# Optimization experiments

Measured on AMD Instinct MI355X. Metric: run time of the kernel, lower is better.

## Reference

```python
import jax, jax.numpy as jnp
import numpy as np

T, D, N, W = 8192, 768, 10000, 32  # tokens, hidden dim, num spans, max span width


def setup_inputs() -> dict:
    key = jax.random.key(0)
    k1, k2, k3, k4, k5 = jax.random.split(key, 5)
    sentence_embeddings = jax.random.normal(k1, (T, D), dtype=jnp.float32)
    lengths = jax.random.randint(k2, (N,), 1, W + 1)           # span lengths in [1, W]
    starts = jax.random.randint(k3, (N,), 0, T - W)
    ends = starts + lengths - 1                                 # inclusive end, < T
    sentence_spans = jnp.stack([starts, ends], axis=1).astype(jnp.int32)
    Wq = (jax.random.normal(k4, (D, D), dtype=jnp.float32) / np.sqrt(D).astype(np.float32))
    bq = jax.random.normal(k5, (D,), dtype=jnp.float32) * 0.01
    return {"sentence_embeddings": sentence_embeddings,
            "sentence_spans": sentence_spans,
            "Wq": Wq, "bq": bq}


def reference(sentence_embeddings, sentence_spans, Wq, bq):
    # Padded + masked batched version of the per-span loop:
    #   span_emb = emb[s:e+1]; q = span_emb @ Wq.T + bq
    #   w = softmax(q @ span_emb.T, dim=1); out = (w @ span_emb).sum(0)
    starts = sentence_spans[:, 0]                               # [N]
    lengths = sentence_spans[:, 1] - starts + 1                 # inclusive end -> length
    offs = jnp.arange(W)
    pos = starts[:, None] + offs[None, :]                       # [N, W] token indices
    valid = offs[None, :] < lengths[:, None]                    # [N, W] in-span mask
    pos = jnp.clip(pos, 0, sentence_embeddings.shape[0] - 1)
    span_emb = sentence_embeddings[pos]                         # [N, W, D] ragged gather
    span_emb = jnp.where(valid[:, :, None], span_emb, 0.0)
    query = jnp.einsum('nwd,ed->nwe', span_emb, Wq) + bq        # [N, W, D]
    scores = jnp.einsum('nqd,nkd->nqk', query, span_emb)        # [N, W, W]
    scores = jnp.where(valid[:, None, :], scores, -jnp.inf)     # mask pad keys (softmax dim=1)
    weights = jax.nn.softmax(scores, axis=-1)
    attn = jnp.einsum('nqk,nkd->nqd', weights, span_emb)        # [N, W, D]
    attn = jnp.where(valid[:, :, None], attn, 0.0)              # drop pad query rows
    return attn.sum(axis=1)                                     # [N, D] == torch.sum(attention, dim=0) per span
```

## Files before the change

### kernel.cpp

```cpp
#include <hip/hip_runtime.h>
#include <hip/hip_bf16.h>
#include <cstddef>
#include <cstdint>

constexpr int Tt = 8192;
constexpr int Dd = 768;
constexpr int Nn = 10000;
constexpr int Ww = 32;

typedef __bf16 bf16x8 __attribute__((ext_vector_type(8)));
typedef __bf16 bf16x4 __attribute__((ext_vector_type(4)));
typedef _Float16 half8v __attribute__((ext_vector_type(8)));
typedef _Float16 half4v __attribute__((ext_vector_type(4)));
typedef float f32x4 __attribute__((ext_vector_type(4)));

#define MFMA16(a, b, c) __builtin_amdgcn_mfma_f32_16x16x32_bf16((a), (b), (c), 0, 0, 0)
#define MFMAH(a, b, c) __builtin_amdgcn_mfma_f32_16x16x32_f16((a), (b), (c), 0, 0, 0)

__global__ __launch_bounds__(256) void conv_f16_kernel(const float* __restrict__ emb,
                                                       const float* __restrict__ Wq,
                                                       _Float16* __restrict__ Ef,
                                                       _Float16* __restrict__ Wf) {
    const int nE = (Tt * Dd) / 4;
    const int nW = (Dd * Dd) / 4;
    const int i = blockIdx.x * 256 + threadIdx.x;
    if (i < nE) {
        const float4 v = reinterpret_cast<const float4*>(emb)[i];
        half4v o;
        o[0] = (_Float16)v.x; o[1] = (_Float16)v.y;
        o[2] = (_Float16)v.z; o[3] = (_Float16)v.w;
        reinterpret_cast<half4v*>(Ef)[i] = o;
    } else {
        const int j = i - nE;
        if (j < nW) {
            const float4 v = reinterpret_cast<const float4*>(Wq)[j];
            half4v o;
            o[0] = (_Float16)v.x; o[1] = (_Float16)v.y;
            o[2] = (_Float16)v.z; o[3] = (_Float16)v.w;
            reinterpret_cast<half4v*>(Wf)[j] = o;
        }
    }
}

template <bool LO>
__global__ __launch_bounds__(256) void conv_kernel(const float* __restrict__ src,
                                                   __bf16* __restrict__ h,
                                                   __bf16* __restrict__ l, int n4) {
    const int i = blockIdx.x * 256 + threadIdx.x;
    if (i >= n4) return;
    const float4 v = reinterpret_cast<const float4*>(src)[i];
    bf16x4 oh, ol;
    oh[0] = (__bf16)v.x; oh[1] = (__bf16)v.y; oh[2] = (__bf16)v.z; oh[3] = (__bf16)v.w;
    reinterpret_cast<bf16x4*>(h)[i] = oh;
    if (LO) {
        ol[0] = (__bf16)(v.x - (float)oh[0]);
        ol[1] = (__bf16)(v.y - (float)oh[1]);
        ol[2] = (__bf16)(v.z - (float)oh[2]);
        ol[3] = (__bf16)(v.w - (float)oh[3]);
        reinterpret_cast<bf16x4*>(l)[i] = ol;
    }
}

__global__ __launch_bounds__(256) void zero_kernel(int* __restrict__ p, int n) {
    const int i = blockIdx.x * 256 + threadIdx.x;
    if (i < n) p[i] = 0;
}

__global__ __launch_bounds__(256) void hist_kernel(const int* __restrict__ spans,
                                                   int* __restrict__ hist) {
    const int i = blockIdx.x * 256 + threadIdx.x;
    if (i < Nn) atomicAdd(&hist[spans[2 * i]], 1);
}

__global__ __launch_bounds__(256) void scan_kernel(int* __restrict__ hist) {
    __shared__ int part[256];
    const int t = threadIdx.x;
    int vals[32];
    int sum = 0;
#pragma unroll
    for (int i = 0; i < 32; ++i) { vals[i] = hist[t * 32 + i]; sum += vals[i]; }
    part[t] = sum;
    __syncthreads();
    for (int off = 1; off < 256; off <<= 1) {
        const int v = (t >= off) ? part[t - off] : 0;
        __syncthreads();
        part[t] += v;
        __syncthreads();
    }
    int run = (t == 0) ? 0 : part[t - 1];
#pragma unroll
    for (int i = 0; i < 32; ++i) { const int v = vals[i]; hist[t * 32 + i] = run; run += v; }
}

__global__ __launch_bounds__(256) void scatter_kernel(const int* __restrict__ spans,
                                                      int* __restrict__ offs,
                                                      int* __restrict__ perm) {
    const int i = blockIdx.x * 256 + threadIdx.x;
    if (i < Nn) {
        const int p = atomicAdd(&offs[spans[2 * i]], 1);
        perm[p] = i;
    }
}

template <bool SPLIT>
__global__ __launch_bounds__(256) void qproj_kernel(const float* __restrict__ emb,
                                                    const float* __restrict__ Wq,
                                                    const float* __restrict__ bq,
                                                    __bf16* __restrict__ Qh,
                                                    __bf16* __restrict__ Ql) {
    __shared__ float As[64][32];
    __shared__ float Bs[64][32];
    const int tid = threadIdx.x;
    const int tx = tid & 15;
    const int ty = tid >> 4;
    const int m0 = blockIdx.x * 64;
    const int n0 = blockIdx.y * 64;

    float acc[4][4] = {};

    for (int kc = 0; kc < Dd; kc += 32) {
#pragma unroll
        for (int i = 0; i < 2; ++i) {
            const int f   = tid + i * 256;
            const int row = f >> 3;
            const int c4  = f & 7;
            const int ph  = (c4 + (row >> 2)) & 7;
            *reinterpret_cast<float4*>(&As[row][ph * 4]) =
                *reinterpret_cast<const float4*>(&emb[(size_t)(m0 + row) * Dd + kc + c4 * 4]);
            *reinterpret_cast<float4*>(&Bs[row][ph * 4]) =
                *reinterpret_cast<const float4*>(&Wq[(size_t)(n0 + row) * Dd + kc + c4 * 4]);
        }
        __syncthreads();
#pragma unroll
        for (int d4 = 0; d4 < 8; ++d4) {
            float4 av[4], bv[4];
#pragma unroll
            for (int r = 0; r < 4; ++r)
                av[r] = *reinterpret_cast<const float4*>(&As[ty * 4 + r][((d4 + ty) & 7) * 4]);
#pragma unroll
            for (int c = 0; c < 4; ++c)
                bv[c] = *reinterpret_cast<const float4*>(&Bs[tx * 4 + c][((d4 + tx) & 7) * 4]);
#pragma unroll
            for (int r = 0; r < 4; ++r)
#pragma unroll
                for (int c = 0; c < 4; ++c) {
                    acc[r][c] += av[r].x * bv[c].x;
                    acc[r][c] += av[r].y * bv[c].y;
                    acc[r][c] += av[r].z * bv[c].z;
                    acc[r][c] += av[r].w * bv[c].w;
                }
        }
        __syncthreads();
    }
#pragma unroll
    for (int r = 0; r < 4; ++r) {
        bf16x4 oh, ol;
#pragma unroll
        for (int c = 0; c < 4; ++c) {
            const float v = acc[r][c] + bq[n0 + tx * 4 + c];
            const __bf16 h = (__bf16)v;
            oh[c] = h;
            if (SPLIT) ol[c] = (__bf16)(v - (float)h);
        }
        const size_t off = (size_t)(m0 + ty * 4 + r) * Dd + n0 + tx * 4;
        *reinterpret_cast<bf16x4*>(&Qh[off]) = oh;
        if (SPLIT) *reinterpret_cast<bf16x4*>(&Ql[off]) = ol;
    }
}

__global__ __launch_bounds__(256) void qproj_f16_kernel(const _Float16* __restrict__ Ef,
                                                        const _Float16* __restrict__ Wf,
                                                        const float* __restrict__ bq,
                                                        _Float16* __restrict__ Qf) {
    __shared__ __align__(16) _Float16 As[128 * 64];
    __shared__ __align__(16) _Float16 Bs[96 * 64];

    const int tid  = threadIdx.x;
    const int wave = tid >> 6;
    const int lane = tid & 63;

    const int b   = blockIdx.x;
    const int xcd = b & 7;
    const int li  = b >> 3;
    const int mt  = xcd * 8 + (li >> 3);
    const int nt  = li & 7;
    const int m0 = mt * 128;
    const int n0 = nt * 96;
    const int wm = (wave & 1) * 64;
    const int wn = (wave >> 1) * 48;
    const int fr = lane & 15;
    const int kg = lane >> 4;

    int ar[4], ao[4];
#pragma unroll
    for (int i = 0; i < 4; ++i) {
        const int s = tid + i * 256;
        ar[i] = s >> 3;
        ao[i] = ((s & 7) ^ (ar[i] & 7)) * 8;
    }
    int br[3], bo[3];
#pragma unroll
    for (int i = 0; i < 3; ++i) {
        const int s = tid + i * 256;
        br[i] = s >> 3;
        bo[i] = ((s & 7) ^ (br[i] & 7)) * 8;
    }

    f32x4 acc[4][3] = {};

    for (int kc = 0; kc < Dd; kc += 64) {
        half8v ra[4], rb[3];
#pragma unroll
        for (int i = 0; i < 4; ++i)
            ra[i] = *reinterpret_cast<const half8v*>(&Ef[(size_t)(m0 + ar[i]) * Dd + kc + ao[i]]);
#pragma unroll
        for (int i = 0; i < 3; ++i)
            rb[i] = *reinterpret_cast<const half8v*>(&Wf[(size_t)(n0 + br[i]) * Dd + kc + bo[i]]);
        __syncthreads();
#pragma unroll
        for (int i = 0; i < 4; ++i)
            *reinterpret_cast<half8v*>(&As[(tid + i * 256) * 8]) = ra[i];
#pragma unroll
        for (int i = 0; i < 3; ++i)
            *reinterpret_cast<half8v*>(&Bs[(tid + i * 256) * 8]) = rb[i];
        __syncthreads();

#pragma unroll
        for (int step = 0; step < 2; ++step) {
            const int g = kg + 4 * step;
            half8v a[4], bb[3];
#pragma unroll
            for (int r = 0; r < 4; ++r) {
                const int R = wm + r * 16 + fr;
                a[r] = *reinterpret_cast<const half8v*>(&As[R * 64 + (g ^ (R & 7)) * 8]);
            }
#pragma unroll
            for (int c = 0; c < 3; ++c) {
                const int R = wn + c * 16 + fr;
                bb[c] = *reinterpret_cast<const half8v*>(&Bs[R * 64 + (g ^ (R & 7)) * 8]);
            }
#pragma unroll
            for (int r = 0; r < 4; ++r)
#pragma unroll
                for (int c = 0; c < 3; ++c)
                    acc[r][c] = MFMAH(a[r], bb[c], acc[r][c]);
        }
    }

#pragma unroll
    for (int c = 0; c < 3; ++c) {
        const int ocol = n0 + wn + c * 16 + fr;
        const float bqv = bq[ocol];
#pragma unroll
        for (int r = 0; r < 4; ++r)
#pragma unroll
            for (int j = 0; j < 4; ++j) {
                const int orow = m0 + wm + r * 16 + kg * 4 + j;
                Qf[(size_t)orow * Dd + ocol] = (_Float16)(acc[r][c][j] + bqv);
            }
    }
}

__global__ __launch_bounds__(256) void span_attn_win_kernel(const _Float16* __restrict__ Ef,
                                                            const int* __restrict__ spans,
                                                            const _Float16* __restrict__ Qf,
                                                            const int* __restrict__ perm,
                                                            float* __restrict__ out) {
    constexpr int WR = 48, CH = 128, ST = 136, NCH = Dd / CH;
    __shared__ __align__(16) _Float16 Qs[WR * ST];
    __shared__ __align__(16) _Float16 Es[WR * ST];

    const int tid  = threadIdx.x;
    const int wave = tid >> 6;
    const int lane = tid & 63;

    const int b     = blockIdx.x;
    const int bp    = (b & 7) * 313 + (b >> 3);
    const int slot0 = bp * 4;
    const int slot  = slot0 + wave;
    const bool active = slot < Nn;

    int s0 = perm[slot0 < Nn ? slot0 : (Nn - 1)];
    if ((unsigned)s0 >= (unsigned)Nn) s0 = 0;
    int s = active ? perm[slot] : s0;
    if ((unsigned)s >= (unsigned)Nn) s = 0;

    const int w0    = spans[2 * s0];
    const int start = spans[2 * s];
    const int L     = spans[2 * s + 1] - start + 1;
    const bool big  = L > 16;
    const int sl    = start - w0;
    const bool inwin = active && sl >= 0 && sl <= (WR - 32);

    const int row = lane & 15;
    const int kq  = lane >> 4;

    const size_t gq = (size_t)(start + row) * Dd + kq * 8;

    f32x4 acc00 = {0.f, 0.f, 0.f, 0.f};
    f32x4 acc01 = {0.f, 0.f, 0.f, 0.f};
    f32x4 acc10 = {0.f, 0.f, 0.f, 0.f};
    f32x4 acc11 = {0.f, 0.f, 0.f, 0.f};

    for (int c = 0; c < NCH; ++c) {
        const int c0 = c * CH;
        __syncthreads();
#pragma unroll
        for (int i = 0; i < 3; ++i) {
            const int seg = tid + i * 256;
            const int r  = seg >> 4;
            const int cs = seg & 15;
            const int gr = w0 + r < Tt ? w0 + r : Tt - 1;
            const size_t ga = (size_t)gr * Dd + c0 + cs * 8;
            *reinterpret_cast<half8v*>(&Qs[r * ST + cs * 8]) =
                *reinterpret_cast<const half8v*>(&Qf[ga]);
            *reinterpret_cast<half8v*>(&Es[r * ST + cs * 8]) =
                *reinterpret_cast<const half8v*>(&Ef[ga]);
        }
        __syncthreads();

        if (inwin) {
            const int ab = (sl + row) * ST + kq * 8;
#pragma unroll
            for (int j = 0; j < 4; ++j) {
                const int o = j * 32;
                const half8v a0 = *reinterpret_cast<const half8v*>(&Qs[ab + o]);
                const half8v b0 = *reinterpret_cast<const half8v*>(&Es[ab + o]);
                acc00 = MFMAH(a0, b0, acc00);
                if (big) {
                    const half8v a1 = *reinterpret_cast<const half8v*>(&Qs[ab + 16 * ST + o]);
                    const half8v b1 = *reinterpret_cast<const half8v*>(&Es[ab + 16 * ST + o]);
                    acc01 = MFMAH(a0, b1, acc01);
                    acc10 = MFMAH(a1, b0, acc10);
                    acc11 = MFMAH(a1, b1, acc11);
                }
            }
        } else if (active) {
#pragma unroll
            for (int j = 0; j < 4; ++j) {
                const int o = c0 + j * 32;
                const half8v a0 = *reinterpret_cast<const half8v*>(&Qf[gq + o]);
                const half8v b0 = *reinterpret_cast<const half8v*>(&Ef[gq + o]);
                acc00 = MFMAH(a0, b0, acc00);
                if (big) {
                    const half8v a1 = *reinterpret_cast<const half8v*>(&Qf[gq + 16 * Dd + o]);
                    const half8v b1 = *reinterpret_cast<const half8v*>(&Ef[gq + 16 * Dd + o]);
                    acc01 = MFMAH(a0, b1, acc01);
                    acc10 = MFMAH(a1, b0, acc10);
                    acc11 = MFMAH(a1, b1, acc11);
                }
            }
        }
    }

    const float NEG = -1e30f;
    const bool kv0 = row < L;
    const bool kv1 = (16 + row) < L;
    float cA, cB;
    {
        float w00[4], w01[4], w10[4], w11[4];
#pragma unroll
        for (int r = 0; r < 4; ++r) {
            float m = kv0 ? acc00[r] : NEG;
            if (big) m = fmaxf(m, kv1 ? acc01[r] : NEG);
#pragma unroll
            for (int st = 1; st <= 8; st <<= 1) m = fmaxf(m, __shfl_xor(m, st));
            const float e0 = kv0 ? __expf(acc00[r] - m) : 0.f;
            const float e1 = (big && kv1) ? __expf(acc01[r] - m) : 0.f;
            float sum = e0 + e1;
#pragma unroll
            for (int st = 1; st <= 8; st <<= 1) sum += __shfl_xor(sum, st);
            const float inv = 1.f / sum;
            const bool qv = (kq * 4 + r) < L;
            w00[r] = qv ? e0 * inv : 0.f;
            w01[r] = qv ? e1 * inv : 0.f;
            if (big) {
                float mh = kv0 ? acc10[r] : NEG;
                mh = fmaxf(mh, kv1 ? acc11[r] : NEG);
#pragma unroll
                for (int st = 1; st <= 8; st <<= 1) mh = fmaxf(mh, __shfl_xor(mh, st));
                const float f0 = kv0 ? __expf(acc10[r] - mh) : 0.f;
                const float f1 = kv1 ? __expf(acc11[r] - mh) : 0.f;
                float sh = f0 + f1;
#pragma unroll
                for (int st = 1; st <= 8; st <<= 1) sh += __shfl_xor(sh, st);
                const float invh = 1.f / sh;
                const bool qvh = (16 + kq * 4 + r) < L;
                w10[r] = qvh ? f0 * invh : 0.f;
                w11[r] = qvh ? f1 * invh : 0.f;
            }
        }
        float pa = w00[0] + w00[1] + w00[2] + w00[3];
        float pb = 0.f;
        if (big) {
            pa += w10[0] + w10[1] + w10[2] + w10[3];
            pb = w01[0] + w01[1] + w01[2] + w01[3] +
                 w11[0] + w11[1] + w11[2] + w11[3];
        }
        pa += __shfl_xor(pa, 16);
        pa += __shfl_xor(pa, 32);
        if (big) {
            pb += __shfl_xor(pb, 16);
            pb += __shfl_xor(pb, 32);
        }
        cA = pa;
        cB = pb;
    }

    if (active) {
        f32x4 o[3] = {};
        const int KP = (L + 3) & ~3;
        const _Float16* ebase = Ef + (size_t)start * Dd + lane * 4;
        for (int k = 0; k < KP; k += 4) {
            float cv[4];
            half4v ev[4][3];
#pragma unroll
            for (int j = 0; j < 4; ++j) {
                const int kk = k + j;
                cv[j] = (kk < 16) ? __shfl(cA, kk) : __shfl(cB, kk - 16);
#pragma unroll
                for (int i = 0; i < 3; ++i)
                    ev[j][i] = *reinterpret_cast<const half4v*>(ebase + (size_t)kk * Dd + i * 256);
            }
#pragma unroll
            for (int j = 0; j < 4; ++j)
#pragma unroll
                for (int i = 0; i < 3; ++i) {
                    o[i][0] += cv[j] * (float)ev[j][i][0];
                    o[i][1] += cv[j] * (float)ev[j][i][1];
                    o[i][2] += cv[j] * (float)ev[j][i][2];
                    o[i][3] += cv[j] * (float)ev[j][i][3];
                }
        }
#pragma unroll
        for (int i = 0; i < 3; ++i)
            *reinterpret_cast<f32x4*>(&out[(size_t)s * Dd + i * 256 + lane * 4]) = o[i];
    }
}

template <bool SPLIT, bool SORTED>
__global__ __launch_bounds__(256) void span_attn_g_kernel(const __bf16* __restrict__ Eb,
                                                          const int* __restrict__ spans,
                                                          const __bf16* __restrict__ Qh,
                                                          const __bf16* __restrict__ Ql,
                                                          const int* __restrict__ perm,
                                                          float* __restrict__ out) {
    const int wave = threadIdx.x >> 6;
    const int lane = threadIdx.x & 63;

    int s;
    bool active;
    if (SORTED) {
        const int b    = blockIdx.x;
        const int bp   = (b & 7) * 313 + (b >> 3);
        const int slot = bp * 4 + wave;
        active = slot < Nn;
        int sv = active ? perm[slot] : 0;
        if ((unsigned)sv >= (unsigned)Nn) sv = 0;
        s = sv;
    } else {
        s = blockIdx.x * 4 + wave;
        active = true;
    }

    const int start = spans[2 * s];
    const int L     = spans[2 * s + 1] - start + 1;
    const bool big  = L > 16;

    const int row = lane & 15;
    const int kq  = lane >> 4;

    const size_t rbase = (size_t)(start + row) * Dd + kq * 8;
    const __bf16* qh0 = Qh + rbase;
    const __bf16* eb0 = Eb + rbase;
    const __bf16* ql0 = SPLIT ? (Ql + rbase) : nullptr;

    f32x4 acc00 = {0.f, 0.f, 0.f, 0.f};
    f32x4 acc01 = {0.f, 0.f, 0.f, 0.f};
    f32x4 acc10 = {0.f, 0.f, 0.f, 0.f};
    f32x4 acc11 = {0.f, 0.f, 0.f, 0.f};

    if (!big) {
        for (int kc = 0; kc < Dd; kc += 128) {
            bf16x8 A[4], B[4], AL[4];
#pragma unroll
            for (int j = 0; j < 4; ++j) {
                const int o = kc + j * 32;
                A[j] = *reinterpret_cast<const bf16x8*>(qh0 + o);
                B[j] = *reinterpret_cast<const bf16x8*>(eb0 + o);
                if (SPLIT) AL[j] = *reinterpret_cast<const bf16x8*>(ql0 + o);
            }
#pragma unroll
            for (int j = 0; j < 4; ++j) {
                acc00 = MFMA16(A[j], B[j], acc00);
                if (SPLIT) acc00 = MFMA16(AL[j], B[j], acc00);
            }
        }
    } else {
        for (int kc = 0; kc < Dd; kc += 64) {
            bf16x8 A0[2], A1[2], B0[2], B1[2], AL0[2], AL1[2];
#pragma unroll
            for (int j = 0; j < 2; ++j) {
                const int o = kc + j * 32;
                A0[j] = *reinterpret_cast<const bf16x8*>(qh0 + o);
                A1[j] = *reinterpret_cast<const bf16x8*>(qh0 + 16 * Dd + o);
                B0[j] = *reinterpret_cast<const bf16x8*>(eb0 + o);
                B1[j] = *reinterpret_cast<const bf16x8*>(eb0 + 16 * Dd + o);
                if (SPLIT) {
                    AL0[j] = *reinterpret_cast<const bf16x8*>(ql0 + o);
                    AL1[j] = *reinterpret_cast<const bf16x8*>(ql0 + 16 * Dd + o);
                }
            }
#pragma unroll
            for (int j = 0; j < 2; ++j) {
                acc00 = MFMA16(A0[j], B0[j], acc00);
                acc01 = MFMA16(A0[j], B1[j], acc01);
                acc10 = MFMA16(A1[j], B0[j], acc10);
                acc11 = MFMA16(A1[j], B1[j], acc11);
                if (SPLIT) {
                    acc00 = MFMA16(AL0[j], B0[j], acc00);
                    acc01 = MFMA16(AL0[j], B1[j], acc01);
                    acc10 = MFMA16(AL1[j], B0[j], acc10);
                    acc11 = MFMA16(AL1[j], B1[j], acc11);
                }
            }
        }
    }

    const float NEG = -1e30f;
    const bool kv0 = row < L;
    const bool kv1 = (16 + row) < L;
    float cA, cB;
    {
        float w00[4], w01[4], w10[4], w11[4];
#pragma unroll
        for (int r = 0; r < 4; ++r) {
            float m = kv0 ? acc00[r] : NEG;
            if (big) m = fmaxf(m, kv1 ? acc01[r] : NEG);
#pragma unroll
            for (int st = 1; st <= 8; st <<= 1) m = fmaxf(m, __shfl_xor(m, st));
            const float e0 = kv0 ? __expf(acc00[r] - m) : 0.f;
            const float e1 = (big && kv1) ? __expf(acc01[r] - m) : 0.f;
            float sum = e0 + e1;
#pragma unroll
            for (int st = 1; st <= 8; st <<= 1) sum += __shfl_xor(sum, st);
            const float inv = 1.f / sum;
            const bool qv = (kq * 4 + r) < L;
            w00[r] = qv ? e0 * inv : 0.f;
            w01[r] = qv ? e1 * inv : 0.f;
            if (big) {
                float mh = kv0 ? acc10[r] : NEG;
                mh = fmaxf(mh, kv1 ? acc11[r] : NEG);
#pragma unroll
                for (int st = 1; st <= 8; st <<= 1) mh = fmaxf(mh, __shfl_xor(mh, st));
                const float f0 = kv0 ? __expf(acc10[r] - mh) : 0.f;
                const float f1 = kv1 ? __expf(acc11[r] - mh) : 0.f;
                float sh = f0 + f1;
#pragma unroll
                for (int st = 1; st <= 8; st <<= 1) sh += __shfl_xor(sh, st);
                const float invh = 1.f / sh;
                const bool qvh = (16 + kq * 4 + r) < L;
                w10[r] = qvh ? f0 * invh : 0.f;
                w11[r] = qvh ? f1 * invh : 0.f;
            }
        }
        float pa = w00[0] + w00[1] + w00[2] + w00[3];
        float pb = 0.f;
        if (big) {
            pa += w10[0] + w10[1] + w10[2] + w10[3];
            pb = w01[0] + w01[1] + w01[2] + w01[3] +
                 w11[0] + w11[1] + w11[2] + w11[3];
        }
        pa += __shfl_xor(pa, 16);
        pa += __shfl_xor(pa, 32);
        if (big) {
            pb += __shfl_xor(pb, 16);
            pb += __shfl_xor(pb, 32);
        }
        cA = pa;
        cB = pb;
    }

    if (active) {
        f32x4 o[3] = {};
        const int KP = (L + 3) & ~3;
        const __bf16* ebase = Eb + (size_t)start * Dd + lane * 4;
        for (int k = 0; k < KP; k += 4) {
            float cv[4];
            bf16x4 ev[4][3];
#pragma unroll
            for (int j = 0; j < 4; ++j) {
                const int kk = k + j;
                cv[j] = (kk < 16) ? __shfl(cA, kk) : __shfl(cB, kk - 16);
#pragma unroll
                for (int i = 0; i < 3; ++i)
                    ev[j][i] = *reinterpret_cast<const bf16x4*>(ebase + (size_t)kk * Dd + i * 256);
            }
#pragma unroll
            for (int j = 0; j < 4; ++j)
#pragma unroll
                for (int i = 0; i < 3; ++i) {
                    o[i][0] += cv[j] * (float)ev[j][i][0];
                    o[i][1] += cv[j] * (float)ev[j][i][1];
                    o[i][2] += cv[j] * (float)ev[j][i][2];
                    o[i][3] += cv[j] * (float)ev[j][i][3];
                }
        }
#pragma unroll
        for (int i = 0; i < 3; ++i)
            *reinterpret_cast<f32x4*>(&out[(size_t)s * Dd + i * 256 + lane * 4]) = o[i];
    }
}

extern "C" void kernel_launch(void* const* d_in, const int* in_sizes, int n_in,
                              void* d_out, int out_size, void* d_ws, size_t ws_size,
                              hipStream_t stream) {
    const float* emb   = (const float*)d_in[0];
    const int*   spans = (const int*)d_in[1];
    const float* Wq    = (const float*)d_in[2];
    const float* bq    = (const float*)d_in[3];
    float*       out   = (float*)d_out;

    const size_t TD = (size_t)Tt * Dd;
    const size_t DD = (size_t)Dd * Dd;
    const size_t intBytes = (size_t)(8192 + 10016) * sizeof(int);
    auto align16 = [](size_t x) { return (x + 15) & ~(size_t)15; };

    const size_t needMain = align16((2 * TD + DD) * 2) + intBytes;
    const size_t needB = align16(3 * TD * 2) + intBytes;
    const size_t needC = 3 * TD * 2;

    if (ws_size >= needMain) {
        char* base = (char*)d_ws;
        _Float16* Qf = (_Float16*)base;
        _Float16* Ef = (_Float16*)(base + TD * 2);
        _Float16* Wf = (_Float16*)(base + 2 * TD * 2);
        int* hist = (int*)(base + align16((2 * TD + DD) * 2));
        int* perm = hist + 8192;

        const int convBlocks = (int)((TD / 4 + DD / 4) / 256);
        conv_f16_kernel<<<convBlocks, 256, 0, stream>>>(emb, Wq, Ef, Wf);
        zero_kernel<<<32, 256, 0, stream>>>(hist, 8192);
        hist_kernel<<<40, 256, 0, stream>>>(spans, hist);
        scan_kernel<<<1, 256, 0, stream>>>(hist);
        scatter_kernel<<<40, 256, 0, stream>>>(spans, hist, perm);
        qproj_f16_kernel<<<512, 256, 0, stream>>>(Ef, Wf, bq, Qf);
        span_attn_win_kernel<<<2504, 256, 0, stream>>>(Ef, spans, Qf, perm, out);
    } else if (ws_size >= needB) {
        __bf16* w = (__bf16*)d_ws;
        __bf16* Qh = w;
        __bf16* Ql = w + TD;
        __bf16* Eh = w + 2 * TD;
        int* hist = (int*)((char*)d_ws + align16(3 * TD * 2));
        int* perm = hist + 8192;

        conv_kernel<false><<<(int)(TD / 4 / 256), 256, 0, stream>>>(emb, Eh, nullptr, (int)(TD / 4));
        zero_kernel<<<32, 256, 0, stream>>>(hist, 8192);
        hist_kernel<<<40, 256, 0, stream>>>(spans, hist);
        scan_kernel<<<1, 256, 0, stream>>>(hist);
        scatter_kernel<<<40, 256, 0, stream>>>(spans, hist, perm);
        qproj_kernel<true><<<dim3(Tt / 64, Dd / 64), 256, 0, stream>>>(emb, Wq, bq, Qh, Ql);
        span_attn_g_kernel<true, true><<<2504, 256, 0, stream>>>(Eh, spans, Qh, Ql, perm, out);
    } else if (ws_size >= needC) {
        __bf16* w = (__bf16*)d_ws;
        __bf16* Qh = w;
        __bf16* Ql = w + TD;
        __bf16* Eh = w + 2 * TD;
        conv_kernel<false><<<(int)(TD / 4 / 256), 256, 0, stream>>>(emb, Eh, nullptr, (int)(TD / 4));
        qproj_kernel<true><<<dim3(Tt / 64, Dd / 64), 256, 0, stream>>>(emb, Wq, bq, Qh, Ql);
        span_attn_g_kernel<true, false><<<2500, 256, 0, stream>>>(Eh, spans, Qh, Ql, nullptr, out);
    } else {
        __bf16* w = (__bf16*)d_ws;
        __bf16* Qh = w;
        __bf16* Eh = w + TD;
        conv_kernel<false><<<(int)(TD / 4 / 256), 256, 0, stream>>>(emb, Eh, nullptr, (int)(TD / 4));
        qproj_kernel<false><<<dim3(Tt / 64, Dd / 64), 256, 0, stream>>>(emb, Wq, bq, Qh, nullptr);
        span_attn_g_kernel<false, false><<<2500, 256, 0, stream>>>(Eh, spans, Qh, nullptr, nullptr, out);
    }
}
```

Baseline: 155.6 us.

## Fuse conversion, span sort and Q projection into one prep kernel

Replaces six prep launches (fp16 conversion, zero, histogram, scan, scatter, Q projection) with a single heterogeneous kernel. Block 0 builds the sorted span permutation in shared memory, blocks 1-512 compute the Q projection directly from fp32 inputs with on-the-fly fp16 conversion, and the remaining blocks convert the embeddings. This removes launch gaps and the separate Wq/E fp16 round trip, at the cost of the GEMM re-reading fp32 data. It also drops the unused intermediate fallback path.

```diff
diff --git a/kernel.cpp b/kernel.cpp
--- a/kernel.cpp
+++ b/kernel.cpp
@@ -17,28 +17,329 @@
 #define MFMA16(a, b, c) __builtin_amdgcn_mfma_f32_16x16x32_bf16((a), (b), (c), 0, 0, 0)
 #define MFMAH(a, b, c) __builtin_amdgcn_mfma_f32_16x16x32_f16((a), (b), (c), 0, 0, 0)
 
-__global__ __launch_bounds__(256) void conv_f16_kernel(const float* __restrict__ emb,
-                                                       const float* __restrict__ Wq,
-                                                       _Float16* __restrict__ Ef,
-                                                       _Float16* __restrict__ Wf) {
-    const int nE = (Tt * Dd) / 4;
-    const int nW = (Dd * Dd) / 4;
-    const int i = blockIdx.x * 256 + threadIdx.x;
-    if (i < nE) {
+__global__ __launch_bounds__(256) void prep_kernel(const float* __restrict__ emb,
+                                                   const float* __restrict__ Wq,
+                                                   const int* __restrict__ spans,
+                                                   const float* __restrict__ bq,
+                                                   _Float16* __restrict__ Ef,
+                                                   _Float16* __restrict__ Qf,
+                                                   int* __restrict__ perm) {
+    __shared__ __align__(16) char smem[33792];
+
+    const int b = blockIdx.x;
+    const int tid = threadIdx.x;
+
+    if (b == 0) {
+        int* hist = (int*)smem;
+        int* part = (int*)(smem + 32768);
+        for (int i = tid; i < 8192; i += 256) hist[i] = 0;
+        __syncthreads();
+        for (int i = tid; i < Nn; i += 256) atomicAdd(&hist[spans[2 * i]], 1);
+        __syncthreads();
+        int vals[32];
+        int sum = 0;
+#pragma unroll
+        for (int i = 0; i < 32; ++i) { vals[i] = hist[tid * 32 + i]; sum += vals[i]; }
+        part[tid] = sum;
+        __syncthreads();
+        for (int off = 1; off < 256; off <<= 1) {
+            const int v = (tid >= off) ? part[tid - off] : 0;
+            __syncthreads();
+            part[tid] += v;
+            __syncthreads();
+        }
+        int run = (tid == 0) ? 0 : part[tid - 1];
+#pragma unroll
+        for (int i = 0; i < 32; ++i) { const int v = vals[i]; hist[tid * 32 + i] = run; run += v; }
+        __syncthreads();
+        for (int i = tid; i < Nn; i += 256) {
+            const int p = atomicAdd(&hist[spans[2 * i]], 1);
+            perm[p] = i;
+        }
+    } else if (b <= 512) {
+        _Float16* As = (_Float16*)smem;
+        _Float16* Bs = (_Float16*)(smem + 16384);
+
+        const int wave = tid >> 6;
+        const int lane = tid & 63;
+
+        const int q  = b & 7;
+        const int j  = (b - 1) >> 3;
+        const int mt = q * 8 + (j >> 3);
+        const int nt = j & 7;
+        const int m0 = mt * 128;
+        const int n0 = nt * 96;
+        const int wm = (wave & 1) * 64;
+        const int wn = (wave >> 1) * 48;
+        const int fr = lane & 15;
+        const int kg = lane >> 4;
+
+        int ar[4], ao[4];
+#pragma unroll
+        for (int i = 0; i < 4; ++i) {
+            const int s = tid + i * 256;
+            ar[i] = s >> 3;
+            ao[i] = ((s & 7) ^ (ar[i] & 7)) * 8;
+        }
+        int br[3], bo[3];
+#pragma unroll
+        for (int i = 0; i < 3; ++i) {
+            const int s = tid + i * 256;
+            br[i] = s >> 3;
+            bo[i] = ((s & 7) ^ (br[i] & 7)) * 8;
+        }
+
+        f32x4 acc[4][3] = {};
+
+        for (int kc = 0; kc < Dd; kc += 64) {
+            half8v ra[4], rb[3];
+#pragma unroll
+            for (int i = 0; i < 4; ++i) {
+                const size_t g = (size_t)(m0 + ar[i]) * Dd + kc + ao[i];
+                const float4 v0 = *reinterpret_cast<const float4*>(&emb[g]);
+                const float4 v1 = *reinterpret_cast<const float4*>(&emb[g + 4]);
+                ra[i][0] = (_Float16)v0.x; ra[i][1] = (_Float16)v0.y;
+                ra[i][2] = (_Float16)v0.z; ra[i][3] = (_Float16)v0.w;
+                ra[i][4] = (_Float16)v1.x; ra[i][5] = (_Float16)v1.y;
+                ra[i][6] = (_Float16)v1.z; ra[i][7] = (_Float16)v1.w;
+            }
+#pragma unroll
+            for (int i = 0; i < 3; ++i) {
+                const size_t g = (size_t)(n0 + br[i]) * Dd + kc + bo[i];
+                const float4 v0 = *reinterpret_cast<const float4*>(&Wq[g]);
+                const float4 v1 = *reinterpret_cast<const float4*>(&Wq[g + 4]);
+                rb[i][0] = (_Float16)v0.x; rb[i][1] = (_Float16)v0.y;
+                rb[i][2] = (_Float16)v0.z; rb[i][3] = (_Float16)v0.w;
+                rb[i][4] = (_Float16)v1.x; rb[i][5] = (_Float16)v1.y;
+                rb[i][6] = (_Float16)v1.z; rb[i][7] = (_Float16)v1.w;
+            }
+            __syncthreads();
+#pragma unroll
+            for (int i = 0; i < 4; ++i)
+                *reinterpret_cast<half8v*>(&As[(tid + i * 256) * 8]) = ra[i];
+#pragma unroll
+            for (int i = 0; i < 3; ++i)
+                *reinterpret_cast<half8v*>(&Bs[(tid + i * 256) * 8]) = rb[i];
+            __syncthreads();
+
+#pragma unroll
+            for (int step = 0; step < 2; ++step) {
+                const int g = kg + 4 * step;
+                half8v a[4], bb[3];
+#pragma unroll
+                for (int r = 0; r < 4; ++r) {
+                    const int R = wm + r * 16 + fr;
+                    a[r] = *reinterpret_cast<const half8v*>(&As[R * 64 + (g ^ (R & 7)) * 8]);
+                }
+#pragma unroll
+                for (int c = 0; c < 3; ++c) {
+                    const int R = wn + c * 16 + fr;
+                    bb[c] = *reinterpret_cast<const half8v*>(&Bs[R * 64 + (g ^ (R & 7)) * 8]);
+                }
+#pragma unroll
+                for (int r = 0; r < 4; ++r)
+#pragma unroll
+                    for (int c = 0; c < 3; ++c)
+                        acc[r][c] = MFMAH(a[r], bb[c], acc[r][c]);
+            }
+        }
+
+#pragma unroll
+        for (int c = 0; c < 3; ++c) {
+            const int ocol = n0 + wn + c * 16 + fr;
+            const float bqv = bq[ocol];
+#pragma unroll
+            for (int r = 0; r < 4; ++r)
+#pragma unroll
+                for (int jj = 0; jj < 4; ++jj) {
+                    const int orow = m0 + wm + r * 16 + kg * 4 + jj;
+                    Qf[(size_t)orow * Dd + ocol] = (_Float16)(acc[r][c][jj] + bqv);
+                }
+        }
+    } else {
+        const int i = (b - 513) * 256 + tid;
         const float4 v = reinterpret_cast<const float4*>(emb)[i];
         half4v o;
         o[0] = (_Float16)v.x; o[1] = (_Float16)v.y;
         o[2] = (_Float16)v.z; o[3] = (_Float16)v.w;
         reinterpret_cast<half4v*>(Ef)[i] = o;
-    } else {
-        const int j = i - nE;
-        if (j < nW) {
-            const float4 v = reinterpret_cast<const float4*>(Wq)[j];
-            half4v o;
-            o[0] = (_Float16)v.x; o[1] = (_Float16)v.y;
-            o[2] = (_Float16)v.z; o[3] = (_Float16)v.w;
-            reinterpret_cast<half4v*>(Wf)[j] = o;
-        }
+    }
+}
+
+__global__ __launch_bounds__(256) void span_attn_win_kernel(const _Float16* __restrict__ Ef,
+                                                            const int* __restrict__ spans,
+                                                            const _Float16* __restrict__ Qf,
+                                                            const int* __restrict__ perm,
+                                                            float* __restrict__ out) {
+    constexpr int WR = 48, CH = 128, ST = 136, NCH = Dd / CH;
+    __shared__ __align__(16) _Float16 Qs[WR * ST];
+    __shared__ __align__(16) _Float16 Es[WR * ST];
+
+    const int tid  = threadIdx.x;
+    const int wave = tid >> 6;
+    const int lane = tid & 63;
+
+    const int b     = blockIdx.x;
+    const int bp    = (b & 7) * 313 + (b >> 3);
+    const int slot0 = bp * 4;
+    const int slot  = slot0 + wave;
+    const bool active = slot < Nn;
+
+    int s0 = perm[slot0 < Nn ? slot0 : (Nn - 1)];
+    if ((unsigned)s0 >= (unsigned)Nn) s0 = 0;
+    int s = active ? perm[slot] : s0;
+    if ((unsigned)s >= (unsigned)Nn) s = 0;
+
+    const int w0    = spans[2 * s0];
+    const int start = spans[2 * s];
+    const int L     = spans[2 * s + 1] - start + 1;
+    const bool big  = L > 16;
+    const int sl    = start - w0;
+    const bool inwin = active && sl >= 0 && sl <= (WR - 32);
+
+    const int row = lane & 15;
+    const int kq  = lane >> 4;
+
+    const size_t gq = (size_t)(start + row) * Dd + kq * 8;
+
+    f32x4 acc00 = {0.f, 0.f, 0.f, 0.f};
+    f32x4 acc01 = {0.f, 0.f, 0.f, 0.f};
+    f32x4 acc10 = {0.f, 0.f, 0.f, 0.f};
+    f32x4 acc11 = {0.f, 0.f, 0.f, 0.f};
+
+    for (int c = 0; c < NCH; ++c) {
+        const int c0 = c * CH;
+        __syncthreads();
+#pragma unroll
+        for (int i = 0; i < 3; ++i) {
+            const int seg = tid + i * 256;
+            const int r  = seg >> 4;
+            const int cs = seg & 15;
+            const int gr = w0 + r < Tt ? w0 + r : Tt - 1;
+            const size_t ga = (size_t)gr * Dd + c0 + cs * 8;
+            *reinterpret_cast<half8v*>(&Qs[r * ST + cs * 8]) =
+                *reinterpret_cast<const half8v*>(&Qf[ga]);
+            *reinterpret_cast<half8v*>(&Es[r * ST + cs * 8]) =
+                *reinterpret_cast<const half8v*>(&Ef[ga]);
+        }
+        __syncthreads();
+
+        if (inwin) {
+            const int ab = (sl + row) * ST + kq * 8;
+#pragma unroll
+            for (int j = 0; j < 4; ++j) {
+                const int o = j * 32;
+                const half8v a0 = *reinterpret_cast<const half8v*>(&Qs[ab + o]);
+                const half8v b0 = *reinterpret_cast<const half8v*>(&Es[ab + o]);
+                acc00 = MFMAH(a0, b0, acc00);
+                if (big) {
+                    const half8v a1 = *reinterpret_cast<const half8v*>(&Qs[ab + 16 * ST + o]);
+                    const half8v b1 = *reinterpret_cast<const half8v*>(&Es[ab + 16 * ST + o]);
+                    acc01 = MFMAH(a0, b1, acc01);
+                    acc10 = MFMAH(a1, b0, acc10);
+                    acc11 = MFMAH(a1, b1, acc11);
+                }
+            }
+        } else if (active) {
+#pragma unroll
+            for (int j = 0; j < 4; ++j) {
+                const int o = c0 + j * 32;
+                const half8v a0 = *reinterpret_cast<const half8v*>(&Qf[gq + o]);
+                const half8v b0 = *reinterpret_cast<const half8v*>(&Ef[gq + o]);
+                acc00 = MFMAH(a0, b0, acc00);
+                if (big) {
+                    const half8v a1 = *reinterpret_cast<const half8v*>(&Qf[gq + 16 * Dd + o]);
+                    const half8v b1 = *reinterpret_cast<const half8v*>(&Ef[gq + 16 * Dd + o]);
+                    acc01 = MFMAH(a0, b1, acc01);
+                    acc10 = MFMAH(a1, b0, acc10);
+                    acc11 = MFMAH(a1, b1, acc11);
+                }
+            }
+        }
+    }
+
+    const float NEG = -1e30f;
+    const bool kv0 = row < L;
+    const bool kv1 = (16 + row) < L;
+    float cA, cB;
+    {
+        float w00[4], w01[4], w10[4], w11[4];
+#pragma unroll
+        for (int r = 0; r < 4; ++r) {
+            float m = kv0 ? acc00[r] : NEG;
+            if (big) m = fmaxf(m, kv1 ? acc01[r] : NEG);
+#pragma unroll
+            for (int st = 1; st <= 8; st <<= 1) m = fmaxf(m, __shfl_xor(m, st));
+            const float e0 = kv0 ? __expf(acc00[r] - m) : 0.f;
+            const float e1 = (big && kv1) ? __expf(acc01[r] - m) : 0.f;
+            float sum = e0 + e1;
+#pragma unroll
+            for (int st = 1; st <= 8; st <<= 1) sum += __shfl_xor(sum, st);
+            const float inv = 1.f / sum;
+            const bool qv = (kq * 4 + r) < L;
+            w00[r] = qv ? e0 * inv : 0.f;
+            w01[r] = qv ? e1 * inv : 0.f;
+            if (big) {
+                float mh = kv0 ? acc10[r] : NEG;
+                mh = fmaxf(mh, kv1 ? acc11[r] : NEG);
+#pragma unroll
+                for (int st = 1; st <= 8; st <<= 1) mh = fmaxf(mh, __shfl_xor(mh, st));
+                const float f0 = kv0 ? __expf(acc10[r] - mh) : 0.f;
+                const float f1 = kv1 ? __expf(acc11[r] - mh) : 0.f;
+                float sh = f0 + f1;
+#pragma unroll
+                for (int st = 1; st <= 8; st <<= 1) sh += __shfl_xor(sh, st);
+                const float invh = 1.f / sh;
+                const bool qvh = (16 + kq * 4 + r) < L;
+                w10[r] = qvh ? f0 * invh : 0.f;
+                w11[r] = qvh ? f1 * invh : 0.f;
+            }
+        }
+        float pa = w00[0] + w00[1] + w00[2] + w00[3];
+        float pb = 0.f;
+        if (big) {
+            pa += w10[0] + w10[1] + w10[2] + w10[3];
+            pb = w01[0] + w01[1] + w01[2] + w01[3] +
+                 w11[0] + w11[1] + w11[2] + w11[3];
+        }
+        pa += __shfl_xor(pa, 16);
+        pa += __shfl_xor(pa, 32);
+        if (big) {
+            pb += __shfl_xor(pb, 16);
+            pb += __shfl_xor(pb, 32);
+        }
+        cA = pa;
+        cB = pb;
+    }
+
+    if (active) {
+        f32x4 o[3] = {};
+        const int KP = (L + 3) & ~3;
+        const _Float16* ebase = Ef + (size_t)start * Dd + lane * 4;
+        for (int k = 0; k < KP; k += 4) {
+            float cv[4];
+            half4v ev[4][3];
+#pragma unroll
+            for (int j = 0; j < 4; ++j) {
+                const int kk = k + j;
+                cv[j] = (kk < 16) ? __shfl(cA, kk) : __shfl(cB, kk - 16);
+#pragma unroll
+                for (int i = 0; i < 3; ++i)
+                    ev[j][i] = *reinterpret_cast<const half4v*>(ebase + (size_t)kk * Dd + i * 256);
+            }
+#pragma unroll
+            for (int j = 0; j < 4; ++j)
+#pragma unroll
+                for (int i = 0; i < 3; ++i) {
+                    o[i][0] += cv[j] * (float)ev[j][i][0];
+                    o[i][1] += cv[j] * (float)ev[j][i][1];
+                    o[i][2] += cv[j] * (float)ev[j][i][2];
+                    o[i][3] += cv[j] * (float)ev[j][i][3];
+                }
+        }
+#pragma unroll
+        for (int i = 0; i < 3; ++i)
+            *reinterpret_cast<f32x4*>(&out[(size_t)s * Dd + i * 256 + lane * 4]) = o[i];
     }
 }
 
@@ -61,47 +362,6 @@
     }
 }
 
-__global__ __launch_bounds__(256) void zero_kernel(int* __restrict__ p, int n) {
-    const int i = blockIdx.x * 256 + threadIdx.x;
-    if (i < n) p[i] = 0;
-}
-
-__global__ __launch_bounds__(256) void hist_kernel(const int* __restrict__ spans,
-                                                   int* __restrict__ hist) {
-    const int i = blockIdx.x * 256 + threadIdx.x;
-    if (i < Nn) atomicAdd(&hist[spans[2 * i]], 1);
-}
-
-__global__ __launch_bounds__(256) void scan_kernel(int* __restrict__ hist) {
-    __shared__ int part[256];
-    const int t = threadIdx.x;
-    int vals[32];
-    int sum = 0;
-#pragma unroll
-    for (int i = 0; i < 32; ++i) { vals[i] = hist[t * 32 + i]; sum += vals[i]; }
-    part[t] = sum;
-    __syncthreads();
-    for (int off = 1; off < 256; off <<= 1) {
-        const int v = (t >= off) ? part[t - off] : 0;
-        __syncthreads();
-        part[t] += v;
-        __syncthreads();
-    }
-    int run = (t == 0) ? 0 : part[t - 1];
-#pragma unroll
-    for (int i = 0; i < 32; ++i) { const int v = vals[i]; hist[t * 32 + i] = run; run += v; }
-}
-
-__global__ __launch_bounds__(256) void scatter_kernel(const int* __restrict__ spans,
-                                                      int* __restrict__ offs,
-                                                      int* __restrict__ perm) {
-    const int i = blockIdx.x * 256 + threadIdx.x;
-    if (i < Nn) {
-        const int p = atomicAdd(&offs[spans[2 * i]], 1);
-        perm[p] = i;
-    }
-}
-
 template <bool SPLIT>
 __global__ __launch_bounds__(256) void qproj_kernel(const float* __restrict__ emb,
                                                     const float* __restrict__ Wq,
@@ -168,187 +428,53 @@
     }
 }
 
-__global__ __launch_bounds__(256) void qproj_f16_kernel(const _Float16* __restrict__ Ef,
-                                                        const _Float16* __restrict__ Wf,
-                                                        const float* __restrict__ bq,
-                                                        _Float16* __restrict__ Qf) {
-    __shared__ __align__(16) _Float16 As[128 * 64];
-    __shared__ __align__(16) _Float16 Bs[96 * 64];
-
-    const int tid  = threadIdx.x;
-    const int wave = tid >> 6;
-    const int lane = tid & 63;
-
-    const int b   = blockIdx.x;
-    const int xcd = b & 7;
-    const int li  = b >> 3;
-    const int mt  = xcd * 8 + (li >> 3);
-    const int nt  = li & 7;
-    const int m0 = mt * 128;
-    const int n0 = nt * 96;
-    const int wm = (wave & 1) * 64;
-    const int wn = (wave >> 1) * 48;
-    const int fr = lane & 15;
-    const int kg = lane >> 4;
-
-    int ar[4], ao[4];
-#pragma unroll
-    for (int i = 0; i < 4; ++i) {
-        const int s = tid + i * 256;
-        ar[i] = s >> 3;
-        ao[i] = ((s & 7) ^ (ar[i] & 7)) * 8;
-    }
-    int br[3], bo[3];
-#pragma unroll
-    for (int i = 0; i < 3; ++i) {
-        const int s = tid + i * 256;
-        br[i] = s >> 3;
-        bo[i] = ((s & 7) ^ (br[i] & 7)) * 8;
-    }
-
-    f32x4 acc[4][3] = {};
-
-    for (int kc = 0; kc < Dd; kc += 64) {
-        half8v ra[4], rb[3];
-#pragma unroll
-        for (int i = 0; i < 4; ++i)
-            ra[i] = *reinterpret_cast<const half8v*>(&Ef[(size_t)(m0 + ar[i]) * Dd + kc + ao[i]]);
-#pragma unroll
-        for (int i = 0; i < 3; ++i)
-            rb[i] = *reinterpret_cast<const half8v*>(&Wf[(size_t)(n0 + br[i]) * Dd + kc + bo[i]]);
-        __syncthreads();
-#pragma unroll
-        for (int i = 0; i < 4; ++i)
-            *reinterpret_cast<half8v*>(&As[(tid + i * 256) * 8]) = ra[i];
-#pragma unroll
-        for (int i = 0; i < 3; ++i)
-            *reinterpret_cast<half8v*>(&Bs[(tid + i * 256) * 8]) = rb[i];
-        __syncthreads();
-
-#pragma unroll
-        for (int step = 0; step < 2; ++step) {
-            const int g = kg + 4 * step;
-            half8v a[4], bb[3];
-#pragma unroll
-            for (int r = 0; r < 4; ++r) {
-                const int R = wm + r * 16 + fr;
-                a[r] = *reinterpret_cast<const half8v*>(&As[R * 64 + (g ^ (R & 7)) * 8]);
-            }
-#pragma unroll
-            for (int c = 0; c < 3; ++c) {
-                const int R = wn + c * 16 + fr;
-                bb[c] = *reinterpret_cast<const half8v*>(&Bs[R * 64 + (g ^ (R & 7)) * 8]);
-            }
-#pragma unroll
-            for (int r = 0; r < 4; ++r)
-#pragma unroll
-                for (int c = 0; c < 3; ++c)
-                    acc[r][c] = MFMAH(a[r], bb[c], acc[r][c]);
-        }
-    }
-
-#pragma unroll
-    for (int c = 0; c < 3; ++c) {
-        const int ocol = n0 + wn + c * 16 + fr;
-        const float bqv = bq[ocol];
-#pragma unroll
-        for (int r = 0; r < 4; ++r)
-#pragma unroll
-            for (int j = 0; j < 4; ++j) {
-                const int orow = m0 + wm + r * 16 + kg * 4 + j;
-                Qf[(size_t)orow * Dd + ocol] = (_Float16)(acc[r][c][j] + bqv);
-            }
-    }
-}
-
-__global__ __launch_bounds__(256) void span_attn_win_kernel(const _Float16* __restrict__ Ef,
-                                                            const int* __restrict__ spans,
-                                                            const _Float16* __restrict__ Qf,
-                                                            const int* __restrict__ perm,
-                                                            float* __restrict__ out) {
-    constexpr int WR = 48, CH = 128, ST = 136, NCH = Dd / CH;
-    __shared__ __align__(16) _Float16 Qs[WR * ST];
-    __shared__ __align__(16) _Float16 Es[WR * ST];
-
-    const int tid  = threadIdx.x;
-    const int wave = tid >> 6;
-    const int lane = tid & 63;
-
-    const int b     = blockIdx.x;
-    const int bp    = (b & 7) * 313 + (b >> 3);
-    const int slot0 = bp * 4;
-    const int slot  = slot0 + wave;
-    const bool active = slot < Nn;
-
-    int s0 = perm[slot0 < Nn ? slot0 : (Nn - 1)];
-    if ((unsigned)s0 >= (unsigned)Nn) s0 = 0;
-    int s = active ? perm[slot] : s0;
-    if ((unsigned)s >= (unsigned)Nn) s = 0;
-
-    const int w0    = spans[2 * s0];
+template <bool SPLIT>
+__global__ __launch_bounds__(256) void span_attn_g_kernel(const __bf16* __restrict__ Eb,
+                                                          const int* __restrict__ spans,
+                                                          const __bf16* __restrict__ Qh,
+                                                          const __bf16* __restrict__ Ql,
+                                                          float* __restrict__ out) {
+    const int wave = threadIdx.x >> 6;
+    const int lane = threadIdx.x & 63;
+    const int s = blockIdx.x * 4 + wave;
+
     const int start = spans[2 * s];
     const int L     = spans[2 * s + 1] - start + 1;
     const bool big  = L > 16;
-    const int sl    = start - w0;
-    const bool inwin = active && sl >= 0 && sl <= (WR - 32);
 
     const int row = lane & 15;
     const int kq  = lane >> 4;
 
-    const size_t gq = (size_t)(start + row) * Dd + kq * 8;
+    const size_t rbase = (size_t)(start + row) * Dd + kq * 8;
+    const __bf16* qh0 = Qh + rbase;
+    const __bf16* eb0 = Eb + rbase;
+    const __bf16* ql0 = SPLIT ? (Ql + rbase) : nullptr;
 
     f32x4 acc00 = {0.f, 0.f, 0.f, 0.f};
     f32x4 acc01 = {0.f, 0.f, 0.f, 0.f};
     f32x4 acc10 = {0.f, 0.f, 0.f, 0.f};
     f32x4 acc11 = {0.f, 0.f, 0.f, 0.f};
 
-    for (int c = 0; c < NCH; ++c) {
-        const int c0 = c * CH;
-        __syncthreads();
-#pragma unroll
-        for (int i = 0; i < 3; ++i) {
-            const int seg = tid + i * 256;
-            const int r  = seg >> 4;
-            const int cs = seg & 15;
-            const int gr = w0 + r < Tt ? w0 + r : Tt - 1;
-            const size_t ga = (size_t)gr * Dd + c0 + cs * 8;
-            *reinterpret_cast<half8v*>(&Qs[r * ST + cs * 8]) =
-                *reinterpret_cast<const half8v*>(&Qf[ga]);
-            *reinterpret_cast<half8v*>(&Es[r * ST + cs * 8]) =
-                *reinterpret_cast<const half8v*>(&Ef[ga]);
-        }
-        __syncthreads();
-
-        if (inwin) {
-            const int ab = (sl + row) * ST + kq * 8;
-#pragma unroll
-            for (int j = 0; j < 4; ++j) {
-                const int o = j * 32;
-                const half8v a0 = *reinterpret_cast<const half8v*>(&Qs[ab + o]);
-                const half8v b0 = *reinterpret_cast<const half8v*>(&Es[ab + o]);
-                acc00 = MFMAH(a0, b0, acc00);
-                if (big) {
-                    const half8v a1 = *reinterpret_cast<const half8v*>(&Qs[ab + 16 * ST + o]);
-                    const half8v b1 = *reinterpret_cast<const half8v*>(&Es[ab + 16 * ST + o]);
-                    acc01 = MFMAH(a0, b1, acc01);
-                    acc10 = MFMAH(a1, b0, acc10);
-                    acc11 = MFMAH(a1, b1, acc11);
-                }
-            }
-        } else if (active) {
-#pragma unroll
-            for (int j = 0; j < 4; ++j) {
-                const int o = c0 + j * 32;
-                const half8v a0 = *reinterpret_cast<const half8v*>(&Qf[gq + o]);
-                const half8v b0 = *reinterpret_cast<const half8v*>(&Ef[gq + o]);
-                acc00 = MFMAH(a0, b0, acc00);
-                if (big) {
-                    const half8v a1 = *reinterpret_cast<const half8v*>(&Qf[gq + 16 * Dd + o]);
-                    const half8v b1 = *reinterpret_cast<const half8v*>(&Ef[gq + 16 * Dd + o]);
-                    acc01 = MFMAH(a0, b1, acc01);
-                    acc10 = MFMAH(a1, b0, acc10);
-                    acc11 = MFMAH(a1, b1, acc11);
-                }
+    for (int kc = 0; kc < Dd; kc += 32) {
+        const bf16x8 a0 = *reinterpret_cast<const bf16x8*>(qh0 + kc);
+        const bf16x8 b0 = *reinterpret_cast<const bf16x8*>(eb0 + kc);
+        acc00 = MFMA16(a0, b0, acc00);
+        bf16x8 al0;
+        if (SPLIT) {
+            al0 = *reinterpret_cast<const bf16x8*>(ql0 + kc);
+            acc00 = MFMA16(al0, b0, acc00);
+        }
+        if (big) {
+            const bf16x8 a1 = *reinterpret_cast<const bf16x8*>(qh0 + 16 * Dd + kc);
+            const bf16x8 b1 = *reinterpret_cast<const bf16x8*>(eb0 + 16 * Dd + kc);
+            acc01 = MFMA16(a0, b1, acc01);
+            acc10 = MFMA16(a1, b0, acc10);
+            acc11 = MFMA16(a1, b1, acc11);
+            if (SPLIT) {
+                const bf16x8 al1 = *reinterpret_cast<const bf16x8*>(ql0 + 16 * Dd + kc);
+                acc01 = MFMA16(al0, b1, acc01);
+                acc10 = MFMA16(al1, b0, acc10);
+                acc11 = MFMA16(al1, b1, acc11);
             }
         }
     }
@@ -407,181 +533,7 @@
         cB = pb;
     }
 
-    if (active) {
-        f32x4 o[3] = {};
-        const int KP = (L + 3) & ~3;
-        const _Float16* ebase = Ef + (size_t)start * Dd + lane * 4;
-        for (int k = 0; k < KP; k += 4) {
-            float cv[4];
-            half4v ev[4][3];
-#pragma unroll
-            for (int j = 0; j < 4; ++j) {
-                const int kk = k + j;
-                cv[j] = (kk < 16) ? __shfl(cA, kk) : __shfl(cB, kk - 16);
-#pragma unroll
-                for (int i = 0; i < 3; ++i)
-                    ev[j][i] = *reinterpret_cast<const half4v*>(ebase + (size_t)kk * Dd + i * 256);
-            }
-#pragma unroll
-            for (int j = 0; j < 4; ++j)
-#pragma unroll
-                for (int i = 0; i < 3; ++i) {
-                    o[i][0] += cv[j] * (float)ev[j][i][0];
-                    o[i][1] += cv[j] * (float)ev[j][i][1];
-                    o[i][2] += cv[j] * (float)ev[j][i][2];
-                    o[i][3] += cv[j] * (float)ev[j][i][3];
-                }
-        }
-#pragma unroll
-        for (int i = 0; i < 3; ++i)
-            *reinterpret_cast<f32x4*>(&out[(size_t)s * Dd + i * 256 + lane * 4]) = o[i];
-    }
-}
-
-template <bool SPLIT, bool SORTED>
-__global__ __launch_bounds__(256) void span_attn_g_kernel(const __bf16* __restrict__ Eb,
-                                                          const int* __restrict__ spans,
-                                                          const __bf16* __restrict__ Qh,
-                                                          const __bf16* __restrict__ Ql,
-                                                          const int* __restrict__ perm,
-                                                          float* __restrict__ out) {
-    const int wave = threadIdx.x >> 6;
-    const int lane = threadIdx.x & 63;
-
-    int s;
-    bool active;
-    if (SORTED) {
-        const int b    = blockIdx.x;
-        const int bp   = (b & 7) * 313 + (b >> 3);
-        const int slot = bp * 4 + wave;
-        active = slot < Nn;
-        int sv = active ? perm[slot] : 0;
-        if ((unsigned)sv >= (unsigned)Nn) sv = 0;
-        s = sv;
-    } else {
-        s = blockIdx.x * 4 + wave;
-        active = true;
-    }
-
-    const int start = spans[2 * s];
-    const int L     = spans[2 * s + 1] - start + 1;
-    const bool big  = L > 16;
-
-    const int row = lane & 15;
-    const int kq  = lane >> 4;
-
-    const size_t rbase = (size_t)(start + row) * Dd + kq * 8;
-    const __bf16* qh0 = Qh + rbase;
-    const __bf16* eb0 = Eb + rbase;
-    const __bf16* ql0 = SPLIT ? (Ql + rbase) : nullptr;
-
-    f32x4 acc00 = {0.f, 0.f, 0.f, 0.f};
-    f32x4 acc01 = {0.f, 0.f, 0.f, 0.f};
-    f32x4 acc10 = {0.f, 0.f, 0.f, 0.f};
-    f32x4 acc11 = {0.f, 0.f, 0.f, 0.f};
-
-    if (!big) {
-        for (int kc = 0; kc < Dd; kc += 128) {
-            bf16x8 A[4], B[4], AL[4];
-#pragma unroll
-            for (int j = 0; j < 4; ++j) {
-                const int o = kc + j * 32;
-                A[j] = *reinterpret_cast<const bf16x8*>(qh0 + o);
-                B[j] = *reinterpret_cast<const bf16x8*>(eb0 + o);
-                if (SPLIT) AL[j] = *reinterpret_cast<const bf16x8*>(ql0 + o);
-            }
-#pragma unroll
-            for (int j = 0; j < 4; ++j) {
-                acc00 = MFMA16(A[j], B[j], acc00);
-                if (SPLIT) acc00 = MFMA16(AL[j], B[j], acc00);
-            }
-        }
-    } else {
-        for (int kc = 0; kc < Dd; kc += 64) {
-            bf16x8 A0[2], A1[2], B0[2], B1[2], AL0[2], AL1[2];
-#pragma unroll
-            for (int j = 0; j < 2; ++j) {
-                const int o = kc + j * 32;
-                A0[j] = *reinterpret_cast<const bf16x8*>(qh0 + o);
-                A1[j] = *reinterpret_cast<const bf16x8*>(qh0 + 16 * Dd + o);
-                B0[j] = *reinterpret_cast<const bf16x8*>(eb0 + o);
-                B1[j] = *reinterpret_cast<const bf16x8*>(eb0 + 16 * Dd + o);
-                if (SPLIT) {
-                    AL0[j] = *reinterpret_cast<const bf16x8*>(ql0 + o);
-                    AL1[j] = *reinterpret_cast<const bf16x8*>(ql0 + 16 * Dd + o);
-                }
-            }
-#pragma unroll
-            for (int j = 0; j < 2; ++j) {
-                acc00 = MFMA16(A0[j], B0[j], acc00);
-                acc01 = MFMA16(A0[j], B1[j], acc01);
-                acc10 = MFMA16(A1[j], B0[j], acc10);
-                acc11 = MFMA16(A1[j], B1[j], acc11);
-                if (SPLIT) {
-                    acc00 = MFMA16(AL0[j], B0[j], acc00);
-                    acc01 = MFMA16(AL0[j], B1[j], acc01);
-                    acc10 = MFMA16(AL1[j], B0[j], acc10);
-                    acc11 = MFMA16(AL1[j], B1[j], acc11);
-                }
-            }
-        }
-    }
-
-    const float NEG = -1e30f;
-    const bool kv0 = row < L;
-    const bool kv1 = (16 + row) < L;
-    float cA, cB;
     {
-        float w00[4], w01[4], w10[4], w11[4];
-#pragma unroll
-        for (int r = 0; r < 4; ++r) {
-            float m = kv0 ? acc00[r] : NEG;
-            if (big) m = fmaxf(m, kv1 ? acc01[r] : NEG);
-#pragma unroll
-            for (int st = 1; st <= 8; st <<= 1) m = fmaxf(m, __shfl_xor(m, st));
-            const float e0 = kv0 ? __expf(acc00[r] - m) : 0.f;
-            const float e1 = (big && kv1) ? __expf(acc01[r] - m) : 0.f;
-            float sum = e0 + e1;
-#pragma unroll
-            for (int st = 1; st <= 8; st <<= 1) sum += __shfl_xor(sum, st);
-            const float inv = 1.f / sum;
-            const bool qv = (kq * 4 + r) < L;
-            w00[r] = qv ? e0 * inv : 0.f;
-            w01[r] = qv ? e1 * inv : 0.f;
-            if (big) {
-                float mh = kv0 ? acc10[r] : NEG;
-                mh = fmaxf(mh, kv1 ? acc11[r] : NEG);
-#pragma unroll
-                for (int st = 1; st <= 8; st <<= 1) mh = fmaxf(mh, __shfl_xor(mh, st));
-                const float f0 = kv0 ? __expf(acc10[r] - mh) : 0.f;
-                const float f1 = kv1 ? __expf(acc11[r] - mh) : 0.f;
-                float sh = f0 + f1;
-#pragma unroll
-                for (int st = 1; st <= 8; st <<= 1) sh += __shfl_xor(sh, st);
-                const float invh = 1.f / sh;
-                const bool qvh = (16 + kq * 4 + r) < L;
-                w10[r] = qvh ? f0 * invh : 0.f;
-                w11[r] = qvh ? f1 * invh : 0.f;
-            }
-        }
-        float pa = w00[0] + w00[1] + w00[2] + w00[3];
-        float pb = 0.f;
-        if (big) {
-            pa += w10[0] + w10[1] + w10[2] + w10[3];
-            pb = w01[0] + w01[1] + w01[2] + w01[3] +
-                 w11[0] + w11[1] + w11[2] + w11[3];
-        }
-        pa += __shfl_xor(pa, 16);
-        pa += __shfl_xor(pa, 32);
-        if (big) {
-            pb += __shfl_xor(pb, 16);
-            pb += __shfl_xor(pb, 32);
-        }
-        cA = pa;
-        cB = pb;
-    }
-
-    if (active) {
         f32x4 o[3] = {};
         const int KP = (L + 3) & ~3;
         const __bf16* ebase = Eb + (size_t)start * Dd + lane * 4;
@@ -622,45 +574,19 @@
     float*       out   = (float*)d_out;
 
     const size_t TD = (size_t)Tt * Dd;
-    const size_t DD = (size_t)Dd * Dd;
-    const size_t intBytes = (size_t)(8192 + 10016) * sizeof(int);
     auto align16 = [](size_t x) { return (x + 15) & ~(size_t)15; };
 
-    const size_t needMain = align16((2 * TD + DD) * 2) + intBytes;
-    const size_t needB = align16(3 * TD * 2) + intBytes;
+    const size_t needMain = align16(2 * TD * 2) + 10016 * sizeof(int);
     const size_t needC = 3 * TD * 2;
 
     if (ws_size >= needMain) {
         char* base = (char*)d_ws;
         _Float16* Qf = (_Float16*)base;
         _Float16* Ef = (_Float16*)(base + TD * 2);
-        _Float16* Wf = (_Float16*)(base + 2 * TD * 2);
-        int* hist = (int*)(base + align16((2 * TD + DD) * 2));
-        int* perm = hist + 8192;
-
-        const int convBlocks = (int)((TD / 4 + DD / 4) / 256);
-        conv_f16_kernel<<<convBlocks, 256, 0, stream>>>(emb, Wq, Ef, Wf);
-        zero_kernel<<<32, 256, 0, stream>>>(hist, 8192);
-        hist_kernel<<<40, 256, 0, stream>>>(spans, hist);
-        scan_kernel<<<1, 256, 0, stream>>>(hist);
-        scatter_kernel<<<40, 256, 0, stream>>>(spans, hist, perm);
-        qproj_f16_kernel<<<512, 256, 0, stream>>>(Ef, Wf, bq, Qf);
+        int* perm = (int*)(base + align16(2 * TD * 2));
+
+        prep_kernel<<<6657, 256, 0, stream>>>(emb, Wq, spans, bq, Ef, Qf, perm);
         span_attn_win_kernel<<<2504, 256, 0, stream>>>(Ef, spans, Qf, perm, out);
-    } else if (ws_size >= needB) {
-        __bf16* w = (__bf16*)d_ws;
-        __bf16* Qh = w;
-        __bf16* Ql = w + TD;
-        __bf16* Eh = w + 2 * TD;
-        int* hist = (int*)((char*)d_ws + align16(3 * TD * 2));
-        int* perm = hist + 8192;
-
-        conv_kernel<false><<<(int)(TD / 4 / 256), 256, 0, stream>>>(emb, Eh, nullptr, (int)(TD / 4));
-        zero_kernel<<<32, 256, 0, stream>>>(hist, 8192);
-        hist_kernel<<<40, 256, 0, stream>>>(spans, hist);
-        scan_kernel<<<1, 256, 0, stream>>>(hist);
-        scatter_kernel<<<40, 256, 0, stream>>>(spans, hist, perm);
-        qproj_kernel<true><<<dim3(Tt / 64, Dd / 64), 256, 0, stream>>>(emb, Wq, bq, Qh, Ql);
-        span_attn_g_kernel<true, true><<<2504, 256, 0, stream>>>(Eh, spans, Qh, Ql, perm, out);
     } else if (ws_size >= needC) {
         __bf16* w = (__bf16*)d_ws;
         __bf16* Qh = w;
@@ -668,13 +594,13 @@
         __bf16* Eh = w + 2 * TD;
         conv_kernel<false><<<(int)(TD / 4 / 256), 256, 0, stream>>>(emb, Eh, nullptr, (int)(TD / 4));
         qproj_kernel<true><<<dim3(Tt / 64, Dd / 64), 256, 0, stream>>>(emb, Wq, bq, Qh, Ql);
-        span_attn_g_kernel<true, false><<<2500, 256, 0, stream>>>(Eh, spans, Qh, Ql, nullptr, out);
+        span_attn_g_kernel<true><<<2500, 256, 0, stream>>>(Eh, spans, Qh, Ql, out);
     } else {
         __bf16* w = (__bf16*)d_ws;
         __bf16* Qh = w;
         __bf16* Eh = w + TD;
         conv_kernel<false><<<(int)(TD / 4 / 256), 256, 0, stream>>>(emb, Eh, nullptr, (int)(TD / 4));
         qproj_kernel<false><<<dim3(Tt / 64, Dd / 64), 256, 0, stream>>>(emb, Wq, bq, Qh, nullptr);
-        span_attn_g_kernel<false, false><<<2500, 256, 0, stream>>>(Eh, spans, Qh, nullptr, nullptr, out);
+        span_attn_g_kernel<false><<<2500, 256, 0, stream>>>(Eh, spans, Qh, nullptr, out);
     }
 }
```

Result: no change. 155.7 us (+0.0%).
